# Kernel optimization log

Measured on AMD Instinct MI355X. Metric: run time of the kernel, lower is better.

The kernel has to match this reference:

```python
import jax, jax.numpy as jnp
import numpy as np
from jax import lax

TOPK = 10
THRESHOLD = 0.5
MARGIN = 0.5
EPS = 1e-8


def setup_inputs() -> dict:
    key = jax.random.key(0)
    k1, k2 = jax.random.split(key)
    B, C, H, W = 8, 256, 128, 128
    loc_features = jax.random.normal(k1, (B, C, H, W), dtype=jnp.float32)
    det_features = jax.random.normal(k2, (B, C, H, W), dtype=jnp.float32)
    return {"loc_features": loc_features, "det_features": det_features}


def _peak_features(fmap):
    """fmap: [C,H,W] -> (feats [TOPK,C], valid [TOPK] bool).
    Peaks = pixels equal to their 3x3 local max with intensity > THRESHOLD,
    sorted by intensity descending, top TOPK (padded with invalid slots)."""
    C, H, W = fmap.shape
    intensity = jnp.sqrt(jnp.sum(fmap * fmap, axis=0))  # [H,W] L2 norm over channels
    pooled = lax.reduce_window(intensity, -jnp.inf, lax.max,
                               (3, 3), (1, 1), 'SAME')
    peak_mask = (intensity == pooled) & (intensity > THRESHOLD)
    masked = jnp.where(peak_mask, intensity, -jnp.inf).reshape(-1)  # [H*W]
    vals, idx = lax.top_k(masked, TOPK)
    valid = jnp.isfinite(vals)  # slots beyond the actual peak count are -inf
    y = idx // W
    x = idx % W
    feats = fmap[:, y, x].T  # [TOPK, C]
    return feats, valid


def _cosine_sim(a, b):
    # a: [Ka,C], b: [Kb,C]; torch.cosine_similarity semantics with eps clamp
    na = jnp.maximum(jnp.linalg.norm(a, axis=-1), EPS)  # [Ka]
    nb = jnp.maximum(jnp.linalg.norm(b, axis=-1), EPS)  # [Kb]
    return (a @ b.T) / (na[:, None] * nb[None, :])


def _per_sample_loss(det_map, loc_map):
    det_f, det_v = _peak_features(det_map)
    loc_f, loc_v = _peak_features(loc_map)
    sim = _cosine_sim(det_f, loc_f)  # [TOPK, TOPK]
    pair_mask = det_v[:, None] & loc_v[None, :]
    n_pairs = jnp.sum(pair_mask)
    loss_sum = jnp.sum(jnp.where(pair_mask, jax.nn.relu(sim - MARGIN), 0.0))
    # torch 'continue' when either side has no peaks -> contributes 0
    return jnp.where(n_pairs > 0, loss_sum / jnp.maximum(n_pairs, 1).astype(sim.dtype), 0.0)


def reference(loc_features, det_features):
    B = loc_features.shape[0]
    losses = jax.vmap(_per_sample_loss)(det_features, loc_features)  # [B]
    return jnp.sum(losses) / B
```

## Files before the change

### kernel.cpp

```cpp
#include <hip/hip_runtime.h>
#include <math.h>

namespace {
constexpr int kB = 8;
constexpr int kC = 256;
constexpr int kH = 128;
constexpr int kW = 128;
constexpr int kHW = kH * kW;
constexpr int kTopK = 10;
constexpr float kThreshold = 0.5f;
constexpr float kMargin = 0.5f;
constexpr float kEps = 1e-8f;
constexpr int kMaps = 2 * kB;
constexpr int kGrpPlanes = 16;
constexpr int kGroups = kC / kGrpPlanes;
}

__global__ __launch_bounds__(512) void sumsq_kernel(
    const float* __restrict__ loc, const float* __restrict__ det,
    float* __restrict__ partial) {
  __shared__ float acc[kHW];
  const int bid = blockIdx.x;
  const int m = bid >> 4;
  const int g = bid & 15;
  const int t = threadIdx.x;
  const int w = t >> 6;
  const int lane = t & 63;
  const float* __restrict__ src = (m < kB) ? loc : det;
  const int b = m & (kB - 1);
  const float* base = src + (size_t)b * kC * kHW +
                      (size_t)(g * kGrpPlanes) * kHW + w * 2048 + lane * 4;
  float* lacc = acc + w * 2048 + lane * 4;

  {
    float4 v[8];
#pragma unroll
    for (int i = 0; i < 8; ++i) v[i] = *(const float4*)(base + i * 256);
    __builtin_amdgcn_sched_barrier(0);
#pragma unroll
    for (int i = 0; i < 8; ++i) {
      float4 o;
      o.x = v[i].x * v[i].x;
      o.y = v[i].y * v[i].y;
      o.z = v[i].z * v[i].z;
      o.w = v[i].w * v[i].w;
      *(float4*)(lacc + i * 256) = o;
    }
  }
  for (int j = 1; j < kGrpPlanes; ++j) {
    const float* pb = base + (size_t)j * kHW;
    float4 v[8];
#pragma unroll
    for (int i = 0; i < 8; ++i) v[i] = *(const float4*)(pb + i * 256);
    __builtin_amdgcn_sched_barrier(0);
#pragma unroll
    for (int i = 0; i < 8; ++i) {
      float4 a = *(const float4*)(lacc + i * 256);
      a.x = fmaf(v[i].x, v[i].x, a.x);
      a.y = fmaf(v[i].y, v[i].y, a.y);
      a.z = fmaf(v[i].z, v[i].z, a.z);
      a.w = fmaf(v[i].w, v[i].w, a.w);
      *(float4*)(lacc + i * 256) = a;
    }
  }
  float* out = partial + ((size_t)m * kGroups + g) * kHW + w * 2048 + lane * 4;
#pragma unroll
  for (int i = 0; i < 8; ++i)
    *(float4*)(out + i * 256) = *(const float4*)(lacc + i * 256);
}

__global__ __launch_bounds__(256) void combine_kernel(
    const float* __restrict__ partial, float* __restrict__ inten) {
  const int gi = blockIdx.x * 256 + threadIdx.x;
  const int m = gi >> 12;
  const int p = (gi & 4095) * 4;
  const float* pp = partial + (size_t)m * kGroups * kHW + p;
  float4 s = {0.f, 0.f, 0.f, 0.f};
#pragma unroll
  for (int g = 0; g < kGroups; ++g) {
    const float4 q = *(const float4*)(pp + (size_t)g * kHW);
    s.x += q.x;
    s.y += q.y;
    s.z += q.z;
    s.w += q.w;
  }
  float4 o = {sqrtf(s.x), sqrtf(s.y), sqrtf(s.z), sqrtf(s.w)};
  *(float4*)(inten + (size_t)m * kHW + p) = o;
}

__global__ __launch_bounds__(1024) void topk_kernel(
    const float* __restrict__ inten, float* __restrict__ tvals,
    int* __restrict__ tidx) {
  const int m = blockIdx.x;
  const int t = threadIdx.x;
  const int w = t >> 6;
  const int lane = t & 63;
  const float* __restrict__ I = inten + (size_t)m * kHW;

  float v[16];
#pragma unroll
  for (int k = 0; k < 16; ++k) {
    const int p = k * 1024 + t;
    const int y = p >> 7;
    const int x = p & (kW - 1);
    const float c0 = I[p];
    float nmax = -INFINITY;
    for (int dy = -1; dy <= 1; ++dy) {
      const int yy = y + dy;
      if (yy < 0 || yy >= kH) continue;
      for (int dx = -1; dx <= 1; ++dx) {
        const int xx = x + dx;
        if (xx < 0 || xx >= kW) continue;
        nmax = fmaxf(nmax, I[yy * kW + xx]);
      }
    }
    const bool peak = (c0 > kThreshold) && (c0 >= nmax);
    v[k] = peak ? c0 : -INFINITY;
  }

  __shared__ float swv[16][kTopK];
  __shared__ int swi[16][kTopK];
  for (int r = 0; r < kTopK; ++r) {
    float bv = v[0];
    int bi = t;
#pragma unroll
    for (int k = 1; k < 16; ++k) {
      const int idx = k * 1024 + t;
      if (v[k] > bv || (v[k] == bv && idx < bi)) { bv = v[k]; bi = idx; }
    }
    for (int off = 1; off < 64; off <<= 1) {
      const float ov = __shfl_xor(bv, off, 64);
      const int oi = __shfl_xor(bi, off, 64);
      if (ov > bv || (ov == bv && oi < bi)) { bv = ov; bi = oi; }
    }
    if (lane == r) { swv[w][r] = bv; swi[w][r] = bi; }
    if ((bi & 1023) == t) v[bi >> 10] = -INFINITY;
  }
  __syncthreads();

  if (w == 0) {
    float cv[3];
    int ci[3];
#pragma unroll
    for (int q = 0; q < 3; ++q) {
      const int s = lane + 64 * q;
      if (s < 16 * kTopK) {
        cv[q] = swv[s / kTopK][s % kTopK];
        ci[q] = swi[s / kTopK][s % kTopK];
      } else {
        cv[q] = -INFINITY;
        ci[q] = 0x7fffffff;
      }
    }
    for (int r = 0; r < kTopK; ++r) {
      float bv = cv[0];
      int bi = ci[0];
#pragma unroll
      for (int q = 1; q < 3; ++q)
        if (cv[q] > bv || (cv[q] == bv && ci[q] < bi)) { bv = cv[q]; bi = ci[q]; }
      for (int off = 1; off < 64; off <<= 1) {
        const float ov = __shfl_xor(bv, off, 64);
        const int oi = __shfl_xor(bi, off, 64);
        if (ov > bv || (ov == bv && oi < bi)) { bv = ov; bi = oi; }
      }
      if (lane == r) {
        tvals[m * kTopK + r] = bv;
        tidx[m * kTopK + r] = bi;
      }
#pragma unroll
      for (int q = 0; q < 3; ++q)
        if (ci[q] == bi) { cv[q] = -INFINITY; ci[q] = 0x7fffffff; }
    }
  }
}

__global__ __launch_bounds__(256) void loss_kernel(
    const float* __restrict__ loc, const float* __restrict__ det,
    const float* __restrict__ tvals, const int* __restrict__ tidx,
    float* __restrict__ losses) {
  const int b = blockIdx.x;
  const int t = threadIdx.x;
  __shared__ float ds[kTopK][kC + 1];
  __shared__ float ls[kTopK][kC + 1];
  __shared__ float s_red[kC];

  float lv[kTopK], dv[kTopK];
  int li[kTopK], di[kTopK];
#pragma unroll
  for (int i = 0; i < kTopK; ++i) {
    lv[i] = tvals[b * kTopK + i];
    li[i] = tidx[b * kTopK + i];
    dv[i] = tvals[(kB + b) * kTopK + i];
    di[i] = tidx[(kB + b) * kTopK + i];
  }
  const float* lb = loc + (size_t)b * kC * kHW + (size_t)t * kHW;
  const float* db = det + (size_t)b * kC * kHW + (size_t)t * kHW;
#pragma unroll
  for (int i = 0; i < kTopK; ++i) {
    ls[i][t] = lb[li[i]];
    ds[i][t] = db[di[i]];
  }
  __syncthreads();

  float contrib = 0.f;
  if (t < kTopK * kTopK) {
    const int i = t / kTopK;
    const int j = t % kTopK;
    const bool valid = (dv[i] > -1e30f) && (lv[j] > -1e30f);
    if (valid) {
      float dot = 0.f;
#pragma unroll 8
      for (int c = 0; c < kC; ++c) dot = fmaf(ds[i][c], ls[j][c], dot);
      const float na = fmaxf(dv[i], kEps);
      const float nb = fmaxf(lv[j], kEps);
      const float sim = dot / (na * nb);
      contrib = fmaxf(sim - kMargin, 0.f);
    }
  }
  s_red[t] = contrib;
  __syncthreads();
  if (t == 0) {
    int nd = 0, nl = 0;
    for (int i = 0; i < kTopK; ++i) {
      nd += (dv[i] > -1e30f) ? 1 : 0;
      nl += (lv[i] > -1e30f) ? 1 : 0;
    }
    float s = 0.f;
    for (int k = 0; k < kTopK * kTopK; ++k) s += s_red[k];
    const int np = nd * nl;
    losses[b] = (np > 0) ? (s / (float)np) : 0.f;
  }
}

__global__ void final_kernel(const float* __restrict__ losses,
                             float* __restrict__ out) {
  if (threadIdx.x == 0 && blockIdx.x == 0) {
    float s = 0.f;
    for (int i = 0; i < kB; ++i) s += losses[i];
    out[0] = s / (float)kB;
  }
}

extern "C" void kernel_launch(void* const* d_in, const int* in_sizes, int n_in,
                              void* d_out, int out_size, void* d_ws,
                              size_t ws_size, hipStream_t stream) {
  const float* loc = (const float*)d_in[0];
  const float* det = (const float*)d_in[1];
  float* out = (float*)d_out;

  float* wsf = (float*)d_ws;
  float* partial = wsf;
  float* inten = partial + (size_t)kMaps * kGroups * kHW;
  float* tvals = inten + (size_t)kMaps * kHW;
  int* tidx = (int*)(tvals + kMaps * kTopK);
  float* losses = (float*)(tidx + kMaps * kTopK);

  sumsq_kernel<<<dim3(kMaps * kGroups), dim3(512), 0, stream>>>(loc, det,
                                                                partial);
  combine_kernel<<<dim3(kMaps * kHW / 4 / 256), dim3(256), 0, stream>>>(
      partial, inten);
  topk_kernel<<<dim3(kMaps), dim3(1024), 0, stream>>>(inten, tvals, tidx);
  loss_kernel<<<dim3(kB), dim3(kC), 0, stream>>>(loc, det, tvals, tidx,
                                                 losses);
  final_kernel<<<dim3(1), dim3(64), 0, stream>>>(losses, out);
}
```

Baseline: 341.1 us.

## Register-accumulate sumsq, fuse combine with banded peak/topk, add merge stage

The sum-of-squares kernel now keeps its accumulators in registers instead of a 64KB shared array, and uses four times as many blocks so occupancy goes up. The separate combine and single-block-per-map top-k kernels are replaced by one banded kernel. Each block sums the group partials for its rows plus halo rows, runs the 3x3 peak test in shared memory and picks a per-band top-10. A small merge kernel then picks the global top-10 per map. This removes the intensity round trip and the low-parallelism 16-block top-k stage, at the cost of rereading halo rows and adding one launch.

```diff
diff --git a/kernel.cpp b/kernel.cpp
--- a/kernel.cpp
+++ b/kernel.cpp
@@ -14,163 +14,185 @@
 constexpr int kMaps = 2 * kB;
 constexpr int kGrpPlanes = 16;
 constexpr int kGroups = kC / kGrpPlanes;
-}
-
-__global__ __launch_bounds__(512) void sumsq_kernel(
+constexpr int kQuarter = kHW / 4;
+constexpr int kBands = 16;
+constexpr int kBandRows = kH / kBands;
+}
+
+__global__ __launch_bounds__(512, 8) void sumsq_kernel(
     const float* __restrict__ loc, const float* __restrict__ det,
     float* __restrict__ partial) {
-  __shared__ float acc[kHW];
   const int bid = blockIdx.x;
-  const int m = bid >> 4;
-  const int g = bid & 15;
+  const int m = bid >> 6;
+  const int g = (bid >> 2) & 15;
+  const int q = bid & 3;
+  const int t = threadIdx.x;
+  const float* __restrict__ src = (m < kB) ? loc : det;
+  const int b = m & (kB - 1);
+  const float* base = src + (size_t)b * kC * kHW +
+                      (size_t)(g * kGrpPlanes) * kHW + q * kQuarter + t * 4;
+  float4 a0 = {0.f, 0.f, 0.f, 0.f};
+  float4 a1 = {0.f, 0.f, 0.f, 0.f};
+  for (int j = 0; j < kGrpPlanes; j += 4) {
+    float4 v[8];
+#pragma unroll
+    for (int jj = 0; jj < 4; ++jj) {
+      const float* pb = base + (size_t)(j + jj) * kHW;
+      v[2 * jj] = *(const float4*)pb;
+      v[2 * jj + 1] = *(const float4*)(pb + 2048);
+    }
+    __builtin_amdgcn_sched_barrier(0);
+#pragma unroll
+    for (int jj = 0; jj < 4; ++jj) {
+      const float4 u = v[2 * jj];
+      const float4 x = v[2 * jj + 1];
+      a0.x = fmaf(u.x, u.x, a0.x);
+      a0.y = fmaf(u.y, u.y, a0.y);
+      a0.z = fmaf(u.z, u.z, a0.z);
+      a0.w = fmaf(u.w, u.w, a0.w);
+      a1.x = fmaf(x.x, x.x, a1.x);
+      a1.y = fmaf(x.y, x.y, a1.y);
+      a1.z = fmaf(x.z, x.z, a1.z);
+      a1.w = fmaf(x.w, x.w, a1.w);
+    }
+  }
+  float* out = partial + ((size_t)m * kGroups + g) * kHW + q * kQuarter + t * 4;
+  *(float4*)out = a0;
+  *(float4*)(out + 2048) = a1;
+}
+
+__global__ __launch_bounds__(256) void peaktop_kernel(
+    const float* __restrict__ partial, float* __restrict__ cvals,
+    int* __restrict__ cidx) {
+  const int m = blockIdx.x >> 4;
+  const int band = blockIdx.x & 15;
+  const int r0 = band * kBandRows;
   const int t = threadIdx.x;
   const int w = t >> 6;
   const int lane = t & 63;
-  const float* __restrict__ src = (m < kB) ? loc : det;
-  const int b = m & (kB - 1);
-  const float* base = src + (size_t)b * kC * kHW +
-                      (size_t)(g * kGrpPlanes) * kHW + w * 2048 + lane * 4;
-  float* lacc = acc + w * 2048 + lane * 4;
-
-  {
-    float4 v[8];
-#pragma unroll
-    for (int i = 0; i < 8; ++i) v[i] = *(const float4*)(base + i * 256);
-    __builtin_amdgcn_sched_barrier(0);
-#pragma unroll
-    for (int i = 0; i < 8; ++i) {
-      float4 o;
-      o.x = v[i].x * v[i].x;
-      o.y = v[i].y * v[i].y;
-      o.z = v[i].z * v[i].z;
-      o.w = v[i].w * v[i].w;
-      *(float4*)(lacc + i * 256) = o;
-    }
-  }
-  for (int j = 1; j < kGrpPlanes; ++j) {
-    const float* pb = base + (size_t)j * kHW;
-    float4 v[8];
-#pragma unroll
-    for (int i = 0; i < 8; ++i) v[i] = *(const float4*)(pb + i * 256);
-    __builtin_amdgcn_sched_barrier(0);
-#pragma unroll
-    for (int i = 0; i < 8; ++i) {
-      float4 a = *(const float4*)(lacc + i * 256);
-      a.x = fmaf(v[i].x, v[i].x, a.x);
-      a.y = fmaf(v[i].y, v[i].y, a.y);
-      a.z = fmaf(v[i].z, v[i].z, a.z);
-      a.w = fmaf(v[i].w, v[i].w, a.w);
-      *(float4*)(lacc + i * 256) = a;
-    }
-  }
-  float* out = partial + ((size_t)m * kGroups + g) * kHW + w * 2048 + lane * 4;
-#pragma unroll
-  for (int i = 0; i < 8; ++i)
-    *(float4*)(out + i * 256) = *(const float4*)(lacc + i * 256);
-}
-
-__global__ __launch_bounds__(256) void combine_kernel(
-    const float* __restrict__ partial, float* __restrict__ inten) {
-  const int gi = blockIdx.x * 256 + threadIdx.x;
-  const int m = gi >> 12;
-  const int p = (gi & 4095) * 4;
-  const float* pp = partial + (size_t)m * kGroups * kHW + p;
-  float4 s = {0.f, 0.f, 0.f, 0.f};
-#pragma unroll
+  __shared__ float ld[kBandRows + 2][kW + 4];
+  __shared__ float swv[4][kTopK];
+  __shared__ int swi[4][kTopK];
+
+  const int prow0 = r0 - 1;
+  float acc[5] = {0.f, 0.f, 0.f, 0.f, 0.f};
+  const float* pbase = partial + (size_t)m * kGroups * kHW + prow0 * kW;
+#pragma unroll 4
   for (int g = 0; g < kGroups; ++g) {
-    const float4 q = *(const float4*)(pp + (size_t)g * kHW);
-    s.x += q.x;
-    s.y += q.y;
-    s.z += q.z;
-    s.w += q.w;
-  }
-  float4 o = {sqrtf(s.x), sqrtf(s.y), sqrtf(s.z), sqrtf(s.w)};
-  *(float4*)(inten + (size_t)m * kHW + p) = o;
-}
-
-__global__ __launch_bounds__(1024) void topk_kernel(
-    const float* __restrict__ inten, float* __restrict__ tvals,
-    int* __restrict__ tidx) {
-  const int m = blockIdx.x;
-  const int t = threadIdx.x;
-  const int w = t >> 6;
-  const int lane = t & 63;
-  const float* __restrict__ I = inten + (size_t)m * kHW;
-
-  float v[16];
-#pragma unroll
-  for (int k = 0; k < 16; ++k) {
-    const int p = k * 1024 + t;
-    const int y = p >> 7;
-    const int x = p & (kW - 1);
-    const float c0 = I[p];
+    const float* pg = pbase + (size_t)g * kHW;
+#pragma unroll
+    for (int i = 0; i < 5; ++i) {
+      const int p = t + 256 * i;
+      const int gr = prow0 + (p >> 7);
+      if (gr >= 0 && gr < kH) acc[i] += pg[p];
+    }
+  }
+#pragma unroll
+  for (int i = 0; i < 5; ++i) {
+    const int p = t + 256 * i;
+    const int gr = prow0 + (p >> 7);
+    ld[p >> 7][p & 127] = (gr >= 0 && gr < kH) ? sqrtf(acc[i]) : -INFINITY;
+  }
+  __syncthreads();
+
+  float cv[4];
+  int ci[4];
+#pragma unroll
+  for (int i = 0; i < 4; ++i) {
+    const int op = t + 256 * i;
+    const int tr = (op >> 7) + 1;
+    const int col = op & 127;
+    const float c0 = ld[tr][col];
     float nmax = -INFINITY;
+#pragma unroll
     for (int dy = -1; dy <= 1; ++dy) {
-      const int yy = y + dy;
-      if (yy < 0 || yy >= kH) continue;
+#pragma unroll
       for (int dx = -1; dx <= 1; ++dx) {
-        const int xx = x + dx;
-        if (xx < 0 || xx >= kW) continue;
-        nmax = fmaxf(nmax, I[yy * kW + xx]);
+        const int xx = col + dx;
+        if (xx >= 0 && xx < kW) nmax = fmaxf(nmax, ld[tr + dy][xx]);
       }
     }
     const bool peak = (c0 > kThreshold) && (c0 >= nmax);
-    v[k] = peak ? c0 : -INFINITY;
-  }
-
-  __shared__ float swv[16][kTopK];
-  __shared__ int swi[16][kTopK];
+    cv[i] = peak ? c0 : -INFINITY;
+    ci[i] = (r0 + (op >> 7)) * kW + col;
+  }
+
   for (int r = 0; r < kTopK; ++r) {
-    float bv = v[0];
-    int bi = t;
-#pragma unroll
-    for (int k = 1; k < 16; ++k) {
-      const int idx = k * 1024 + t;
-      if (v[k] > bv || (v[k] == bv && idx < bi)) { bv = v[k]; bi = idx; }
-    }
+    float bv = cv[0];
+    int bi = ci[0];
+#pragma unroll
+    for (int i = 1; i < 4; ++i)
+      if (cv[i] > bv || (cv[i] == bv && ci[i] < bi)) { bv = cv[i]; bi = ci[i]; }
     for (int off = 1; off < 64; off <<= 1) {
       const float ov = __shfl_xor(bv, off, 64);
       const int oi = __shfl_xor(bi, off, 64);
       if (ov > bv || (ov == bv && oi < bi)) { bv = ov; bi = oi; }
     }
     if (lane == r) { swv[w][r] = bv; swi[w][r] = bi; }
-    if ((bi & 1023) == t) v[bi >> 10] = -INFINITY;
+#pragma unroll
+    for (int i = 0; i < 4; ++i)
+      if (ci[i] == bi) cv[i] = -INFINITY;
   }
   __syncthreads();
 
   if (w == 0) {
-    float cv[3];
-    int ci[3];
-#pragma unroll
-    for (int q = 0; q < 3; ++q) {
-      const int s = lane + 64 * q;
-      if (s < 16 * kTopK) {
-        cv[q] = swv[s / kTopK][s % kTopK];
-        ci[q] = swi[s / kTopK][s % kTopK];
-      } else {
-        cv[q] = -INFINITY;
-        ci[q] = 0x7fffffff;
-      }
-    }
+    float v0 = -INFINITY;
+    int i0 = 0x7fffffff;
+    if (lane < 4 * kTopK) { v0 = swv[lane / kTopK][lane % kTopK];
+                            i0 = swi[lane / kTopK][lane % kTopK]; }
     for (int r = 0; r < kTopK; ++r) {
-      float bv = cv[0];
-      int bi = ci[0];
-#pragma unroll
-      for (int q = 1; q < 3; ++q)
-        if (cv[q] > bv || (cv[q] == bv && ci[q] < bi)) { bv = cv[q]; bi = ci[q]; }
+      float bv = v0;
+      int bi = i0;
       for (int off = 1; off < 64; off <<= 1) {
         const float ov = __shfl_xor(bv, off, 64);
         const int oi = __shfl_xor(bi, off, 64);
         if (ov > bv || (ov == bv && oi < bi)) { bv = ov; bi = oi; }
       }
       if (lane == r) {
-        tvals[m * kTopK + r] = bv;
-        tidx[m * kTopK + r] = bi;
+        cvals[(m * kBands + band) * kTopK + r] = bv;
+        cidx[(m * kBands + band) * kTopK + r] = bi;
       }
-#pragma unroll
-      for (int q = 0; q < 3; ++q)
-        if (ci[q] == bi) { cv[q] = -INFINITY; ci[q] = 0x7fffffff; }
-    }
+      if (i0 == bi) { v0 = -INFINITY; i0 = 0x7fffffff; }
+    }
+  }
+}
+
+__global__ __launch_bounds__(64) void merge_kernel(
+    const float* __restrict__ cvals, const int* __restrict__ cidx,
+    float* __restrict__ tvals, int* __restrict__ tidx) {
+  const int m = blockIdx.x;
+  const int lane = threadIdx.x;
+  float cv[3];
+  int ci[3];
+#pragma unroll
+  for (int q = 0; q < 3; ++q) {
+    const int s = lane + 64 * q;
+    if (s < kBands * kTopK) {
+      cv[q] = cvals[m * kBands * kTopK + s];
+      ci[q] = cidx[m * kBands * kTopK + s];
+    } else {
+      cv[q] = -INFINITY;
+      ci[q] = 0x7fffffff;
+    }
+  }
+  for (int r = 0; r < kTopK; ++r) {
+    float bv = cv[0];
+    int bi = ci[0];
+#pragma unroll
+    for (int q = 1; q < 3; ++q)
+      if (cv[q] > bv || (cv[q] == bv && ci[q] < bi)) { bv = cv[q]; bi = ci[q]; }
+    for (int off = 1; off < 64; off <<= 1) {
+      const float ov = __shfl_xor(bv, off, 64);
+      const int oi = __shfl_xor(bi, off, 64);
+      if (ov > bv || (ov == bv && oi < bi)) { bv = ov; bi = oi; }
+    }
+    if (lane == r) {
+      tvals[m * kTopK + r] = bv;
+      tidx[m * kTopK + r] = bi;
+    }
+#pragma unroll
+    for (int q = 0; q < 3; ++q)
+      if (ci[q] == bi) { cv[q] = -INFINITY; ci[q] = 0x7fffffff; }
   }
 }
 
@@ -250,16 +272,17 @@
 
   float* wsf = (float*)d_ws;
   float* partial = wsf;
-  float* inten = partial + (size_t)kMaps * kGroups * kHW;
-  float* tvals = inten + (size_t)kMaps * kHW;
+  float* cvals = partial + (size_t)kMaps * kGroups * kHW;
+  int* cidx = (int*)(cvals + kMaps * kBands * kTopK);
+  float* tvals = (float*)(cidx + kMaps * kBands * kTopK);
   int* tidx = (int*)(tvals + kMaps * kTopK);
   float* losses = (float*)(tidx + kMaps * kTopK);
 
-  sumsq_kernel<<<dim3(kMaps * kGroups), dim3(512), 0, stream>>>(loc, det,
-                                                                partial);
-  combine_kernel<<<dim3(kMaps * kHW / 4 / 256), dim3(256), 0, stream>>>(
-      partial, inten);
-  topk_kernel<<<dim3(kMaps), dim3(1024), 0, stream>>>(inten, tvals, tidx);
+  sumsq_kernel<<<dim3(kMaps * kGroups * 4), dim3(512), 0, stream>>>(loc, det,
+                                                                    partial);
+  peaktop_kernel<<<dim3(kMaps * kBands), dim3(256), 0, stream>>>(partial,
+                                                                 cvals, cidx);
+  merge_kernel<<<dim3(kMaps), dim3(64), 0, stream>>>(cvals, cidx, tvals, tidx);
   loss_kernel<<<dim3(kB), dim3(kC), 0, stream>>>(loc, det, tvals, tidx,
                                                  losses);
   final_kernel<<<dim3(1), dim3(64), 0, stream>>>(losses, out);
```

Result: no change. 337.0 us (-1.2%).
